# Kernel optimization log

Hardware: AMD Instinct MI355X
Metric: run time of the kernel (lower is better)

## Reference

```python
import jax, jax.numpy as jnp
import numpy as np

ALPHA = 0.2       # LeakyReLU negative slope
NEG_INF = -9e15   # matches torch's -9000000000000000.0 masking constant


def setup_inputs() -> dict:
    key = jax.random.key(0)
    k1, k2, k3, k4 = jax.random.split(key, 4)
    N, Cin, T, V = 16, 64, 512, 64   # in_channels == out_channels == V == C (forced by module math)
    x = jax.random.normal(k1, (N, Cin, T, V), dtype=jnp.float32)
    # K=3 adjacency partitions with 0/1 entries; forward sums over dim 0 and masks where sum > 0
    A = jax.random.randint(k2, (3, V, V), 0, 2).astype(jnp.float32)
    # learned params (xavier-ish scale)
    W = jax.random.normal(k3, (V, V), dtype=jnp.float32) * 0.15
    a = jax.random.normal(k4, (2 * Cin, 1), dtype=jnp.float32) * 0.15
    return {"x": x, "A": A, "W": W, "a": a}


def reference(x, A, W, a):
    # x: [N, C, T, V_in]; W contracts the vertex dim (last axis), as in torch.matmul(x, W)
    x = jnp.einsum('nctv,vu->nctu', x, W)
    N, C, T, V = x.shape
    xf = x.transpose(0, 2, 3, 1).reshape(N * T, V, C)   # [B, V, C], B = N*T
    Asum = jnp.sum(A, axis=0)                           # [V, V]
    # e[b,i,j] = leakyrelu(cat(x_i, x_j) @ a) = leakyrelu(x_i@a1 + x_j@a2)
    a1, a2 = a[:C, 0], a[C:, 0]                         # [C], [C]
    f = xf @ a1                                         # [B, V]
    g = xf @ a2                                         # [B, V]
    e = jax.nn.leaky_relu(f[:, :, None] + g[:, None, :], ALPHA)  # [B, V, V]
    att = jnp.where(Asum[None, :, :] > 0, e, NEG_INF)
    att = jax.nn.softmax(att, axis=2)
    # dropout is identity in eval mode
    out = jnp.einsum('bij,bjc->bic', att, xf)           # [B, V, C]
    return out.reshape(N, T, V, C).transpose(0, 3, 1, 2)  # [N, C, T, V]
```

## Files before the change

kernel.cpp:

```cpp
#include <hip/hip_runtime.h>
#include <hip/hip_bf16.h>


using bf16x8 = __attribute__((ext_vector_type(8))) short;
using f32x4  = __attribute__((ext_vector_type(4))) float;
typedef unsigned long long ull;

constexpr float ALPHA = 0.2f;

__device__ __forceinline__ unsigned short f2bf(float f) {
    union { __hip_bfloat16 h; unsigned short s; } u;
    u.h = __float2bfloat16(f);
    return u.s;
}

__global__ void prep_kernel(const float* __restrict__ A,
                            const float* __restrict__ W,
                            unsigned short* __restrict__ Wt,
                            ull* __restrict__ mask) {
    __shared__ unsigned short part[64][4];
    const int tid = threadIdx.x;
    {
        const int v = tid & 63, q = tid >> 6;
        #pragma unroll 4
        for (int m = 0; m < 16; ++m) {
            const int u = 16 * q + m;
            Wt[v * 64 + u] = f2bf(W[u * 64 + v]);
        }
    }
    {
        const int i = tid >> 2, q = tid & 3;
        const float4* a0 = (const float4*)(A + i * 64 + q * 16);
        const float4* a1 = (const float4*)(A + 4096 + i * 64 + q * 16);
        const float4* a2 = (const float4*)(A + 8192 + i * 64 + q * 16);
        unsigned m16 = 0;
        #pragma unroll
        for (int j4 = 0; j4 < 4; ++j4) {
            float4 s0 = a0[j4], s1 = a1[j4], s2 = a2[j4];
            if (s0.x + s1.x + s2.x > 0.f) m16 |= 1u << (4 * j4 + 0);
            if (s0.y + s1.y + s2.y > 0.f) m16 |= 1u << (4 * j4 + 1);
            if (s0.z + s1.z + s2.z > 0.f) m16 |= 1u << (4 * j4 + 2);
            if (s0.w + s1.w + s2.w > 0.f) m16 |= 1u << (4 * j4 + 3);
        }
        part[i][q] = (unsigned short)m16;
    }
    __syncthreads();
    if (tid < 64) {
        ull m = (ull)part[tid][0] | ((ull)part[tid][1] << 16)
              | ((ull)part[tid][2] << 32) | ((ull)part[tid][3] << 48);
        mask[tid] = m;
    }
}

__global__ __launch_bounds__(256, 6) void gat_kernel(
    const float* __restrict__ x,
    const float* __restrict__ a,
    const ull* __restrict__ maskbits,
    const unsigned short* __restrict__ Wt,
    float* __restrict__ out)
{
    __shared__ unsigned short XbYb[64 * 72];
    __shared__ unsigned short WtPb[64 * 72];
    __shared__ float al[128];
    __shared__ float fpart[4][64];
    __shared__ float gpart[4][64];
    __shared__ ull ml[64];

    const int tid  = threadIdx.x;
    const int b    = blockIdx.x;
    const int n    = b >> 9, t = b & 511;
    const int w    = tid >> 6, lane = tid & 63;
    const int fr   = lane & 15;
    const int hi   = lane >> 4;
    const int fk   = hi * 8;

    {
        const int c = tid >> 2, q = tid & 3;
        const float* xp = x + (size_t)n * 2097152 + (size_t)c * 32768 + (size_t)t * 64 + q * 16;
        float4 v0 = ((const float4*)xp)[0];
        float4 v1 = ((const float4*)xp)[1];
        float4 v2 = ((const float4*)xp)[2];
        float4 v3 = ((const float4*)xp)[3];
        union { bf16x8 v; unsigned short s[8]; } u0, u1;
        u0.s[0]=f2bf(v0.x); u0.s[1]=f2bf(v0.y); u0.s[2]=f2bf(v0.z); u0.s[3]=f2bf(v0.w);
        u0.s[4]=f2bf(v1.x); u0.s[5]=f2bf(v1.y); u0.s[6]=f2bf(v1.z); u0.s[7]=f2bf(v1.w);
        u1.s[0]=f2bf(v2.x); u1.s[1]=f2bf(v2.y); u1.s[2]=f2bf(v2.z); u1.s[3]=f2bf(v2.w);
        u1.s[4]=f2bf(v3.x); u1.s[5]=f2bf(v3.y); u1.s[6]=f2bf(v3.z); u1.s[7]=f2bf(v3.w);
        *(bf16x8*)&XbYb[c * 72 + q * 16]     = u0.v;
        *(bf16x8*)&XbYb[c * 72 + q * 16 + 8] = u1.v;
    }
    #pragma unroll
    for (int p = 0; p < 2; ++p) {
        const int r  = (tid >> 3) + 32 * p;
        const int cc = (tid & 7) * 8;
        *(bf16x8*)&WtPb[r * 72 + cc] = *(const bf16x8*)&Wt[r * 64 + cc];
    }
    if (tid < 128) al[tid] = a[tid];
    if (tid >= 192) ml[tid - 192] = maskbits[tid - 192];
    __syncthreads();

    {
        f32x4 acc[4] = {{0,0,0,0},{0,0,0,0},{0,0,0,0},{0,0,0,0}};
        #pragma unroll
        for (int kc = 0; kc < 2; ++kc) {
            bf16x8 af = *(const bf16x8*)&XbYb[(16 * w + fr) * 72 + 32 * kc + fk];
            #pragma unroll
            for (int cb = 0; cb < 4; ++cb) {
                bf16x8 bfr = *(const bf16x8*)&WtPb[(16 * cb + fr) * 72 + 32 * kc + fk];
                acc[cb] = __builtin_amdgcn_mfma_f32_16x16x32_bf16(af, bfr, acc[cb], 0, 0, 0);
            }
        }
        float a1r[4], a2r[4];
        #pragma unroll
        for (int r = 0; r < 4; ++r) {
            a1r[r] = al[16 * w + 4 * hi + r];
            a2r[r] = al[64 + 16 * w + 4 * hi + r];
        }
        #pragma unroll
        for (int cb = 0; cb < 4; ++cb) {
            #pragma unroll
            for (int r = 0; r < 4; ++r)
                XbYb[(16 * w + 4 * hi + r) * 72 + 16 * cb + fr] = f2bf(acc[cb][r]);
            float F = acc[cb][0]*a1r[0] + acc[cb][1]*a1r[1] + acc[cb][2]*a1r[2] + acc[cb][3]*a1r[3];
            float G = acc[cb][0]*a2r[0] + acc[cb][1]*a2r[1] + acc[cb][2]*a2r[2] + acc[cb][3]*a2r[3];
            F += __shfl_xor(F, 16, 64); F += __shfl_xor(F, 32, 64);
            G += __shfl_xor(G, 16, 64); G += __shfl_xor(G, 32, 64);
            if (lane < 16) {
                fpart[w][16 * cb + lane] = F;
                gpart[w][16 * cb + lane] = G;
            }
        }
    }
    __syncthreads();

    {
        const float gj = (gpart[0][lane] + gpart[1][lane]) + (gpart[2][lane] + gpart[3][lane]);
        #pragma unroll 4
        for (int k = 0; k < 16; ++k) {
            const int i = 4 * k + w;
            const ull mi = ml[i];
            const float fi = (fpart[0][i] + fpart[1][i]) + (fpart[2][i] + fpart[3][i]);
            const float s0 = fi + gj;
            const float e  = fmaxf(s0, ALPHA * s0);
            float p;
            if (mi == 0ull) p = 1.0f;
            else            p = ((mi >> lane) & 1ull) ? __expf(e) : 0.0f;
            WtPb[i * 72 + lane] = f2bf(p);
        }
    }
    __syncthreads();

    {
        f32x4 acc2[4] = {{0,0,0,0},{0,0,0,0},{0,0,0,0},{0,0,0,0}};
        f32x4 accS[4] = {{0,0,0,0},{0,0,0,0},{0,0,0,0},{0,0,0,0}};
        union { bf16x8 v; unsigned short s[8]; } ones;
        #pragma unroll
        for (int j = 0; j < 8; ++j) ones.s[j] = 0x3f80;
        #pragma unroll
        for (int kc = 0; kc < 2; ++kc) {
            bf16x8 af = *(const bf16x8*)&XbYb[(16 * w + fr) * 72 + 32 * kc + fk];
            #pragma unroll
            for (int cb = 0; cb < 4; ++cb) {
                bf16x8 bfr = *(const bf16x8*)&WtPb[(16 * cb + fr) * 72 + 32 * kc + fk];
                acc2[cb] = __builtin_amdgcn_mfma_f32_16x16x32_bf16(af, bfr, acc2[cb], 0, 0, 0);
                accS[cb] = __builtin_amdgcn_mfma_f32_16x16x32_bf16(ones.v, bfr, accS[cb], 0, 0, 0);
            }
        }
        float* op = out + (size_t)n * 2097152 + (size_t)t * 64;
        #pragma unroll
        for (int cb = 0; cb < 4; ++cb) {
            const float rs  = __builtin_amdgcn_rcpf(accS[cb][0]);
            const int   col = 16 * cb + fr;
            #pragma unroll
            for (int r = 0; r < 4; ++r) {
                const int row = 16 * w + 4 * hi + r;
                op[(size_t)row * 32768 + col] = acc2[cb][r] * rs;
            }
        }
    }
}

extern "C" void kernel_launch(void* const* d_in, const int* in_sizes, int n_in,
                              void* d_out, int out_size, void* d_ws, size_t ws_size,
                              hipStream_t stream) {
    const float* x = (const float*)d_in[0];
    const float* A = (const float*)d_in[1];
    const float* W = (const float*)d_in[2];
    const float* a = (const float*)d_in[3];
    float* out = (float*)d_out;
    unsigned short* Wt = (unsigned short*)d_ws;
    ull* mask = (ull*)((char*)d_ws + 8192);

    prep_kernel<<<1, 256, 0, stream>>>(A, W, Wt, mask);
    gat_kernel<<<16 * 512, 256, 0, stream>>>(x, a, mask, Wt, out);
}
```

Before: 54.24 us.

## Load W fragments and attention params into registers, transpose mask for per-lane bits

Each block now reads its W bf16 MFMA fragments and a1/a2 straight from global memory into registers instead of staging them through shared memory, which removes one LDS buffer and the staging stores. The prep kernel also produces a transposed mask and a row-is-empty bitmask, so each lane holds its own column mask in a register. The f row values are broadcast with readlane instead of being re-summed from shared memory. The goal is less LDS traffic and lower setup latency per block, at the cost of more VGPRs and redundant global or L2 reads of W in every block.

```diff
diff --git a/kernel.cpp b/kernel.cpp
--- a/kernel.cpp
+++ b/kernel.cpp
@@ -17,8 +17,10 @@
 __global__ void prep_kernel(const float* __restrict__ A,
                             const float* __restrict__ W,
                             unsigned short* __restrict__ Wt,
-                            ull* __restrict__ mask) {
+                            ull* __restrict__ maskT,
+                            ull* __restrict__ rowzero) {
     __shared__ unsigned short part[64][4];
+    __shared__ ull rowm[64];
     const int tid = threadIdx.x;
     {
         const int v = tid & 63, q = tid >> 6;
@@ -48,23 +50,30 @@
     if (tid < 64) {
         ull m = (ull)part[tid][0] | ((ull)part[tid][1] << 16)
               | ((ull)part[tid][2] << 32) | ((ull)part[tid][3] << 48);
-        mask[tid] = m;
+        rowm[tid] = m;
+        ull bz = __ballot(m == 0ull);
+        if (tid == 0) rowzero[0] = bz;
+    }
+    __syncthreads();
+    if (tid < 64) {
+        ull mt = 0;
+        for (int i = 0; i < 64; ++i) mt |= ((rowm[i] >> tid) & 1ull) << i;
+        maskT[tid] = mt;
     }
 }
 
 __global__ __launch_bounds__(256, 6) void gat_kernel(
     const float* __restrict__ x,
     const float* __restrict__ a,
-    const ull* __restrict__ maskbits,
     const unsigned short* __restrict__ Wt,
+    const ull* __restrict__ maskT,
+    const ull* __restrict__ rowzero_p,
     float* __restrict__ out)
 {
     __shared__ unsigned short XbYb[64 * 72];
-    __shared__ unsigned short WtPb[64 * 72];
-    __shared__ float al[128];
+    __shared__ unsigned short Pb[64 * 72];
     __shared__ float fpart[4][64];
     __shared__ float gpart[4][64];
-    __shared__ ull ml[64];
 
     const int tid  = threadIdx.x;
     const int b    = blockIdx.x;
@@ -73,6 +82,18 @@
     const int fr   = lane & 15;
     const int hi   = lane >> 4;
     const int fk   = hi * 8;
+
+    const ull mT = maskT[lane];
+    const ull rz = rowzero_p[0];
+
+    const float4 a1v = *(const float4*)&a[16 * w + 4 * hi];
+    const float4 a2v = *(const float4*)&a[64 + 16 * w + 4 * hi];
+    bf16x8 bw[4][2];
+    #pragma unroll
+    for (int cb = 0; cb < 4; ++cb)
+        #pragma unroll
+        for (int kc = 0; kc < 2; ++kc)
+            bw[cb][kc] = *(const bf16x8*)&Wt[(16 * cb + fr) * 64 + 32 * kc + fk];
 
     {
         const int c = tid >> 2, q = tid & 3;
@@ -89,14 +110,6 @@
         *(bf16x8*)&XbYb[c * 72 + q * 16]     = u0.v;
         *(bf16x8*)&XbYb[c * 72 + q * 16 + 8] = u1.v;
     }
-    #pragma unroll
-    for (int p = 0; p < 2; ++p) {
-        const int r  = (tid >> 3) + 32 * p;
-        const int cc = (tid & 7) * 8;
-        *(bf16x8*)&WtPb[r * 72 + cc] = *(const bf16x8*)&Wt[r * 64 + cc];
-    }
-    if (tid < 128) al[tid] = a[tid];
-    if (tid >= 192) ml[tid - 192] = maskbits[tid - 192];
     __syncthreads();
 
     {
@@ -105,24 +118,16 @@
         for (int kc = 0; kc < 2; ++kc) {
             bf16x8 af = *(const bf16x8*)&XbYb[(16 * w + fr) * 72 + 32 * kc + fk];
             #pragma unroll
-            for (int cb = 0; cb < 4; ++cb) {
-                bf16x8 bfr = *(const bf16x8*)&WtPb[(16 * cb + fr) * 72 + 32 * kc + fk];
-                acc[cb] = __builtin_amdgcn_mfma_f32_16x16x32_bf16(af, bfr, acc[cb], 0, 0, 0);
-            }
-        }
-        float a1r[4], a2r[4];
-        #pragma unroll
-        for (int r = 0; r < 4; ++r) {
-            a1r[r] = al[16 * w + 4 * hi + r];
-            a2r[r] = al[64 + 16 * w + 4 * hi + r];
+            for (int cb = 0; cb < 4; ++cb)
+                acc[cb] = __builtin_amdgcn_mfma_f32_16x16x32_bf16(af, bw[cb][kc], acc[cb], 0, 0, 0);
         }
         #pragma unroll
         for (int cb = 0; cb < 4; ++cb) {
             #pragma unroll
             for (int r = 0; r < 4; ++r)
                 XbYb[(16 * w + 4 * hi + r) * 72 + 16 * cb + fr] = f2bf(acc[cb][r]);
-            float F = acc[cb][0]*a1r[0] + acc[cb][1]*a1r[1] + acc[cb][2]*a1r[2] + acc[cb][3]*a1r[3];
-            float G = acc[cb][0]*a2r[0] + acc[cb][1]*a2r[1] + acc[cb][2]*a2r[2] + acc[cb][3]*a2r[3];
+            float F = acc[cb][0]*a1v.x + acc[cb][1]*a1v.y + acc[cb][2]*a1v.z + acc[cb][3]*a1v.w;
+            float G = acc[cb][0]*a2v.x + acc[cb][1]*a2v.y + acc[cb][2]*a2v.z + acc[cb][3]*a2v.w;
             F += __shfl_xor(F, 16, 64); F += __shfl_xor(F, 32, 64);
             G += __shfl_xor(G, 16, 64); G += __shfl_xor(G, 32, 64);
             if (lane < 16) {
@@ -135,17 +140,19 @@
 
     {
         const float gj = (gpart[0][lane] + gpart[1][lane]) + (gpart[2][lane] + gpart[3][lane]);
-        #pragma unroll 4
+        const int myv = 16 * w + fr;
+        const float ftot = (fpart[0][myv] + fpart[1][myv]) + (fpart[2][myv] + fpart[3][myv]);
+        #pragma unroll
         for (int k = 0; k < 16; ++k) {
-            const int i = 4 * k + w;
-            const ull mi = ml[i];
-            const float fi = (fpart[0][i] + fpart[1][i]) + (fpart[2][i] + fpart[3][i]);
+            const int i = 16 * w + k;
+            const float fi = __int_as_float(
+                __builtin_amdgcn_readlane(__float_as_int(ftot), k));
             const float s0 = fi + gj;
             const float e  = fmaxf(s0, ALPHA * s0);
-            float p;
-            if (mi == 0ull) p = 1.0f;
-            else            p = ((mi >> lane) & 1ull) ? __expf(e) : 0.0f;
-            WtPb[i * 72 + lane] = f2bf(p);
+            const bool keep = (mT >> i) & 1ull;
+            const bool zrow = (rz >> i) & 1ull;
+            const float p = zrow ? 1.0f : (keep ? __expf(e) : 0.0f);
+            Pb[i * 72 + lane] = f2bf(p);
         }
     }
     __syncthreads();
@@ -161,7 +168,7 @@
             bf16x8 af = *(const bf16x8*)&XbYb[(16 * w + fr) * 72 + 32 * kc + fk];
             #pragma unroll
             for (int cb = 0; cb < 4; ++cb) {
-                bf16x8 bfr = *(const bf16x8*)&WtPb[(16 * cb + fr) * 72 + 32 * kc + fk];
+                bf16x8 bfr = *(const bf16x8*)&Pb[(16 * cb + fr) * 72 + 32 * kc + fk];
                 acc2[cb] = __builtin_amdgcn_mfma_f32_16x16x32_bf16(af, bfr, acc2[cb], 0, 0, 0);
                 accS[cb] = __builtin_amdgcn_mfma_f32_16x16x32_bf16(ones.v, bfr, accS[cb], 0, 0, 0);
             }
@@ -189,8 +196,9 @@
     const float* a = (const float*)d_in[3];
     float* out = (float*)d_out;
     unsigned short* Wt = (unsigned short*)d_ws;
-    ull* mask = (ull*)((char*)d_ws + 8192);
-
-    prep_kernel<<<1, 256, 0, stream>>>(A, W, Wt, mask);
-    gat_kernel<<<16 * 512, 256, 0, stream>>>(x, a, mask, Wt, out);
-}
+    ull* maskT   = (ull*)((char*)d_ws + 8192);
+    ull* rowzero = (ull*)((char*)d_ws + 8704);
+
+    prep_kernel<<<1, 256, 0, stream>>>(A, W, Wt, maskT, rowzero);
+    gat_kernel<<<16 * 512, 256, 0, stream>>>(x, a, Wt, maskT, rowzero, out);
+}
```

Result: slower. 64.10 us (+18.2%).
